# Kernel tuning notes

Measured on AMD Instinct MI355X. Metric: run time of the kernel, lower is better.

The kernel has to match this reference:

```python
import jax, jax.numpy as jnp
import numpy as np

N, E = 50000, 800000
D, DE = 128, 64
BN_EPS = 1e-5


def _bn(h, gamma, beta):
    # BatchNorm1d in training mode: biased batch statistics over the node axis
    mu = jnp.mean(h, axis=0)
    var = jnp.var(h, axis=0)
    return (h - mu) * jax.lax.rsqrt(var + BN_EPS) * gamma + beta


def setup_inputs() -> dict:
    key = jax.random.key(0)
    ks = jax.random.split(key, 12)
    s = lambda d: 1.0 / np.sqrt(d)
    return {
        "x": jax.random.normal(ks[0], (N, D), jnp.float32),
        "edge_index": jax.random.randint(ks[1], (2, E), 0, N, jnp.int64),
        "edge_attr_processed": jax.random.normal(ks[2], (E, DE), jnp.float32),
        # GINEConv edge linear: edge_dim -> node_dim
        "We": jax.random.uniform(ks[3], (D, DE), jnp.float32, -s(DE), s(DE)),
        "be": jnp.zeros((D,), jnp.float32),
        # MLP: Linear(D, 2D) -> BN(2D) -> ReLU -> Linear(2D, D)
        "W1": jax.random.uniform(ks[4], (2 * D, D), jnp.float32, -s(D), s(D)),
        "b1": jnp.zeros((2 * D,), jnp.float32),
        "g1": jnp.ones((2 * D,), jnp.float32),
        "beta1": jnp.zeros((2 * D,), jnp.float32),
        "W2": jax.random.uniform(ks[5], (D, 2 * D), jnp.float32, -s(2 * D), s(2 * D)),
        "b2": jnp.zeros((D,), jnp.float32),
        # outer BatchNorm(D)
        "g2": jnp.ones((D,), jnp.float32),
        "beta2": jnp.zeros((D,), jnp.float32),
        # GINE trainable eps (init 0.0)
        "eps": jnp.zeros((), jnp.float32),
    }


def reference(x, edge_index, edge_attr_processed, We, be, W1, b1, g1, beta1,
              W2, b2, g2, beta2, eps):
    src, dst = edge_index[0], edge_index[1]
    # GINEConv message: ReLU(x_j + Lin(edge_attr)); gather + edge add + relu
    msg = jax.nn.relu(x[src] + edge_attr_processed @ We.T + be)  # [E, D]
    # scatter-add aggregation at destination nodes
    agg = jax.ops.segment_sum(msg, dst, num_segments=x.shape[0])  # [N, D]
    h = (1.0 + eps) * x + agg
    # MLP: Linear -> BN -> ReLU -> Linear
    h = jax.nn.relu(_bn(h @ W1.T + b1, g1, beta1)) @ W2.T + b2
    # outer BN -> ReLU (dropout is identity at inference)
    return jax.nn.relu(_bn(h, g2, beta2))
```

## Files before the change

### kernel.cpp

```cpp
#include <hip/hip_runtime.h>
#include <stdint.h>
#include <stddef.h>


#define NN 50000
#define EE 800000
#define DD 128
#define DE 64
#define H1 256
#define NGRP 3125

typedef __attribute__((ext_vector_type(8))) short short8;
typedef __attribute__((ext_vector_type(4))) float floatx4;

__device__ __forceinline__ short f2bf(float f) {
    union { float f; uint32_t u; } v; v.f = f;
    return (short)((v.u + 0x7FFFu + ((v.u >> 16) & 1u)) >> 16);
}
__device__ __forceinline__ float bf2f(uint16_t u) {
    union { uint32_t u; float f; } v; v.u = (uint32_t)u << 16;
    return v.f;
}

__global__ __launch_bounds__(256) void swz_kernel(const float* __restrict__ src,
                                                  short* __restrict__ dst,
                                                  int KC, int K, int total) {
    int idx = blockIdx.x * 256 + threadIdx.x;
    if (idx >= total) return;
    int j = idx & 7;
    int lane = (idx >> 3) & 63;
    int f = idx >> 9;
    int kc = f % KC;
    int nt = f / KC;
    int n = nt * 16 + (lane & 15);
    int k = kc * 32 + ((lane >> 4) & 3) * 8 + j;
    dst[idx] = f2bf(src[(size_t)n * K + k]);
}

__global__ __launch_bounds__(256) void count_kernel(const int* __restrict__ ei,
                                                    uint32_t* __restrict__ deg) {
    int e = blockIdx.x * 256 + threadIdx.x;
    atomicAdd(&deg[ei[EE + e]], 1u);
}

__global__ __launch_bounds__(256) void scan1_kernel(const uint32_t* __restrict__ deg,
                                                    uint32_t* __restrict__ partial) {
    __shared__ uint32_t ls[256];
    int i = blockIdx.x * 256 + threadIdx.x;
    ls[threadIdx.x] = (i < NN) ? deg[i] : 0u;
    __syncthreads();
    for (int s = 128; s > 0; s >>= 1) {
        if (threadIdx.x < s) ls[threadIdx.x] += ls[threadIdx.x + s];
        __syncthreads();
    }
    if (threadIdx.x == 0) partial[blockIdx.x] = ls[0];
}

__global__ __launch_bounds__(256) void scan2_kernel(uint32_t* __restrict__ partial) {
    __shared__ uint32_t ls[196];
    if (threadIdx.x < 196) ls[threadIdx.x] = partial[threadIdx.x];
    __syncthreads();
    if (threadIdx.x == 0) {
        uint32_t run = 0;
        for (int i = 0; i < 196; ++i) { uint32_t t = ls[i]; ls[i] = run; run += t; }
    }
    __syncthreads();
    if (threadIdx.x < 196) partial[threadIdx.x] = ls[threadIdx.x];
}

__global__ __launch_bounds__(256) void scan3_kernel(const uint32_t* __restrict__ deg,
                                                    const uint32_t* __restrict__ partial,
                                                    uint32_t* __restrict__ base,
                                                    uint32_t* __restrict__ cursor) {
    __shared__ uint32_t ls[256];
    int i = blockIdx.x * 256 + threadIdx.x;
    uint32_t v = (i < NN) ? deg[i] : 0u;
    ls[threadIdx.x] = v;
    __syncthreads();
    for (int off = 1; off < 256; off <<= 1) {
        uint32_t t = (threadIdx.x >= off) ? ls[threadIdx.x - off] : 0u;
        __syncthreads();
        ls[threadIdx.x] += t;
        __syncthreads();
    }
    if (i < NN) {
        uint32_t b = partial[blockIdx.x] + ls[threadIdx.x] - v;
        base[i] = b;
        cursor[i] = b;
    }
}

__global__ __launch_bounds__(256) void pos_kernel(const int* __restrict__ ei,
                                                  uint32_t* __restrict__ cursor,
                                                  uint32_t* __restrict__ pos) {
    int e = blockIdx.x * 256 + threadIdx.x;
    pos[e] = atomicAdd(&cursor[ei[EE + e]], 1u);
}

#define EDGE_GPW 5
__global__ __launch_bounds__(256) void edge_kernel(
    const float* __restrict__ x,
    const int* __restrict__ ei,
    const float* __restrict__ ea,
    const short* __restrict__ weswz,
    const float* __restrict__ be,
    const uint32_t* __restrict__ pos,
    uint16_t* __restrict__ msg)
{
    const int wave = threadIdx.x >> 6;
    const int lane = threadIdx.x & 63;
    const int l16 = lane & 15;
    const int q = lane >> 4;

    const short8* wp = (const short8*)weswz;
    short8 bfr[16];
#pragma unroll
    for (int f = 0; f < 16; ++f) bfr[f] = wp[f * 64 + lane];
    float bev[8];
#pragma unroll
    for (int t = 0; t < 8; ++t) bev[t] = be[t * 16 + l16];

    const int gbase = (blockIdx.x * 4 + wave) * EDGE_GPW;
    for (int g = 0; g < EDGE_GPW; ++g) {
        const int e0 = (gbase + g) * 16;
        const float* earow = ea + (size_t)(e0 + l16) * DE + q * 8;
        floatx4 p0 = *(const floatx4*)(earow);
        floatx4 p1 = *(const floatx4*)(earow + 4);
        floatx4 p2 = *(const floatx4*)(earow + 32);
        floatx4 p3 = *(const floatx4*)(earow + 36);
        short8 af0, af1;
#pragma unroll
        for (int j = 0; j < 4; ++j) {
            af0[j]     = f2bf(p0[j]);
            af0[j + 4] = f2bf(p1[j]);
            af1[j]     = f2bf(p2[j]);
            af1[j + 4] = f2bf(p3[j]);
        }
        floatx4 acc[8];
#pragma unroll
        for (int t = 0; t < 8; ++t) {
            floatx4 z = {0.f, 0.f, 0.f, 0.f};
            z = __builtin_amdgcn_mfma_f32_16x16x32_bf16(af0, bfr[t * 2], z, 0, 0, 0);
            acc[t] = __builtin_amdgcn_mfma_f32_16x16x32_bf16(af1, bfr[t * 2 + 1], z, 0, 0, 0);
        }
#pragma unroll
        for (int r = 0; r < 4; ++r) {
            const int e = e0 + q * 4 + r;
            const int s = ei[e];
            const uint32_t p = pos[e];
            const float* xr = x + (size_t)s * DD;
            uint16_t* mrow = msg + (size_t)p * DD;
#pragma unroll
            for (int t = 0; t < 8; ++t) {
                float v = acc[t][r] + bev[t] + xr[t * 16 + l16];
                v = fmaxf(v, 0.f);
                mrow[t * 16 + l16] = (uint16_t)f2bf(v);
            }
        }
    }
}

__global__ __launch_bounds__(256) void reduce_kernel(
    const uint16_t* __restrict__ msg,
    const uint32_t* __restrict__ base,
    const uint32_t* __restrict__ deg,
    const float* __restrict__ x,
    const float* __restrict__ epsp,
    float* __restrict__ h)
{
    const int n = blockIdx.x * 4 + (threadIdx.x >> 6);
    const int lane = threadIdx.x & 63;
    const uint32_t* mp = (const uint32_t*)msg + (size_t)base[n] * 64 + lane;
    const uint32_t d = deg[n];
    float s0 = 0.f, s1 = 0.f;
    for (uint32_t i = 0; i < d; ++i) {
        uint32_t u = mp[(size_t)i * 64];
        s0 += bf2f((uint16_t)(u & 0xFFFFu));
        s1 += bf2f((uint16_t)(u >> 16));
    }
    const float c1 = 1.0f + epsp[0];
    const int idx = n * DD + lane * 2;
    float2 xv = *(const float2*)(x + idx);
    float2 o; o.x = c1 * xv.x + s0; o.y = c1 * xv.y + s1;
    *(float2*)(h + idx) = o;
}

__global__ __launch_bounds__(256) void gemm1_kernel(
    const float* __restrict__ h,
    const short* __restrict__ w1swz,
    const float* __restrict__ b1,
    float* __restrict__ t1,
    float* __restrict__ gsum,
    float* __restrict__ gsq)
{
    __shared__ float ls[H1];
    __shared__ float ls2[H1];
    const int tid = threadIdx.x;
    ls[tid] = 0.f; ls2[tid] = 0.f;
    __syncthreads();

    const int wave = tid >> 6;
    const int lane = tid & 63;
    const int l16 = lane & 15;
    const int q = lane >> 4;
    const short8* wp = (const short8*)w1swz;

    const int grp = blockIdx.x * 4 + wave;
    if (grp < NGRP) {
        const int n0 = grp * 16;
        const float* hr = h + (size_t)(n0 + l16) * DD + q * 8;
        short8 af[4];
#pragma unroll
        for (int kc = 0; kc < 4; ++kc) {
            floatx4 va = *(const floatx4*)(hr + kc * 32);
            floatx4 vb = *(const floatx4*)(hr + kc * 32 + 4);
#pragma unroll
            for (int j = 0; j < 4; ++j) {
                af[kc][j]     = f2bf(va[j]);
                af[kc][j + 4] = f2bf(vb[j]);
            }
        }
#pragma unroll
        for (int nt = 0; nt < 16; ++nt) {
            floatx4 acc = {0.f, 0.f, 0.f, 0.f};
#pragma unroll
            for (int kc = 0; kc < 4; ++kc)
                acc = __builtin_amdgcn_mfma_f32_16x16x32_bf16(
                    af[kc], wp[(nt * 4 + kc) * 64 + lane], acc, 0, 0, 0);
            const float bb = b1[nt * 16 + l16];
            float s = 0.f, s2 = 0.f;
#pragma unroll
            for (int r = 0; r < 4; ++r) {
                float v = acc[r] + bb;
                t1[(size_t)(n0 + q * 4 + r) * H1 + nt * 16 + l16] = v;
                s += v; s2 += v * v;
            }
            atomicAdd(&ls[nt * 16 + l16], s);
            atomicAdd(&ls2[nt * 16 + l16], s2);
        }
    }
    __syncthreads();
    atomicAdd(&gsum[tid], ls[tid]);
    atomicAdd(&gsq[tid], ls2[tid]);
}

__global__ __launch_bounds__(256) void gemm2_kernel(
    const float* __restrict__ t1,
    const float* __restrict__ scale1,
    const float* __restrict__ shift1,
    const short* __restrict__ w2swz,
    const float* __restrict__ b2,
    float* __restrict__ h2,
    float* __restrict__ gsum,
    float* __restrict__ gsq)
{
    __shared__ float ls[DD];
    __shared__ float ls2[DD];
    const int tid = threadIdx.x;
    if (tid < DD) { ls[tid] = 0.f; ls2[tid] = 0.f; }
    __syncthreads();

    const int wave = tid >> 6;
    const int lane = tid & 63;
    const int l16 = lane & 15;
    const int q = lane >> 4;
    const short8* wp = (const short8*)w2swz;

    const int grp = blockIdx.x * 4 + wave;
    if (grp < NGRP) {
        const int n0 = grp * 16;
        const float* tr = t1 + (size_t)(n0 + l16) * H1 + q * 8;
        floatx4 acc[8];
#pragma unroll
        for (int nt = 0; nt < 8; ++nt) acc[nt] = (floatx4){0.f, 0.f, 0.f, 0.f};
#pragma unroll
        for (int kc = 0; kc < 8; ++kc) {
            floatx4 va = *(const floatx4*)(tr + kc * 32);
            floatx4 vb = *(const floatx4*)(tr + kc * 32 + 4);
            const int kb = kc * 32 + q * 8;
            short8 af;
#pragma unroll
            for (int j = 0; j < 4; ++j) {
                float u = va[j] * scale1[kb + j] + shift1[kb + j];
                af[j] = f2bf(fmaxf(u, 0.f));
                float w = vb[j] * scale1[kb + 4 + j] + shift1[kb + 4 + j];
                af[j + 4] = f2bf(fmaxf(w, 0.f));
            }
#pragma unroll
            for (int nt = 0; nt < 8; ++nt)
                acc[nt] = __builtin_amdgcn_mfma_f32_16x16x32_bf16(
                    af, wp[(nt * 8 + kc) * 64 + lane], acc[nt], 0, 0, 0);
        }
#pragma unroll
        for (int nt = 0; nt < 8; ++nt) {
            const float bb = b2[nt * 16 + l16];
            float s = 0.f, s2 = 0.f;
#pragma unroll
            for (int r = 0; r < 4; ++r) {
                float v = acc[nt][r] + bb;
                h2[(size_t)(n0 + q * 4 + r) * DD + nt * 16 + l16] = v;
                s += v; s2 += v * v;
            }
            atomicAdd(&ls[nt * 16 + l16], s);
            atomicAdd(&ls2[nt * 16 + l16], s2);
        }
    }
    __syncthreads();
    if (tid < DD) {
        atomicAdd(&gsum[tid], ls[tid]);
        atomicAdd(&gsq[tid], ls2[tid]);
    }
}

__global__ void finalize_kernel(const float* __restrict__ ssum,
                                const float* __restrict__ ssumsq,
                                const float* __restrict__ gamma,
                                const float* __restrict__ beta,
                                float* __restrict__ scale,
                                float* __restrict__ shift, int C) {
    int c = threadIdx.x;
    if (c >= C) return;
    float mu = ssum[c] * (1.0f / NN);
    float var = ssumsq[c] * (1.0f / NN) - mu * mu;
    float rs = rsqrtf(var + 1e-5f);
    float sc = gamma[c] * rs;
    scale[c] = sc;
    shift[c] = beta[c] - mu * sc;
}

__global__ __launch_bounds__(256) void out_kernel(const float* __restrict__ h2,
                                                  const float* __restrict__ scale2,
                                                  const float* __restrict__ shift2,
                                                  float* __restrict__ out) {
    int idx = blockIdx.x * 256 + threadIdx.x;
    int base = idx * 4;
    if (base >= NN * DD) return;
    int c = base & (DD - 1);
    floatx4 v = *(const floatx4*)(h2 + base);
    floatx4 sc = *(const floatx4*)(scale2 + c);
    floatx4 sh = *(const floatx4*)(shift2 + c);
    floatx4 o;
#pragma unroll
    for (int j = 0; j < 4; ++j) o[j] = fmaxf(v[j] * sc[j] + sh[j], 0.f);
    *(floatx4*)(out + base) = o;
}

extern "C" void kernel_launch(void* const* d_in, const int* in_sizes, int n_in,
                              void* d_out, int out_size, void* d_ws, size_t ws_size,
                              hipStream_t stream) {
    const float* x     = (const float*)d_in[0];
    const int*   ei    = (const int*)d_in[1];
    const float* ea    = (const float*)d_in[2];
    const float* We    = (const float*)d_in[3];
    const float* be    = (const float*)d_in[4];
    const float* W1    = (const float*)d_in[5];
    const float* b1    = (const float*)d_in[6];
    const float* g1    = (const float*)d_in[7];
    const float* beta1 = (const float*)d_in[8];
    const float* W2    = (const float*)d_in[9];
    const float* b2    = (const float*)d_in[10];
    const float* g2    = (const float*)d_in[11];
    const float* beta2 = (const float*)d_in[12];
    const float* epsp  = (const float*)d_in[13];

    float* ws      = (float*)d_ws;
    float* gsum1   = ws + 0;
    float* gsq1    = ws + 256;
    float* gsum2   = ws + 512;
    float* gsq2    = ws + 640;
    float* scale1  = ws + 768;
    float* shift1  = ws + 1024;
    float* scale2  = ws + 1280;
    float* shift2  = ws + 1408;
    uint32_t* deg     = (uint32_t*)(ws + 1536);
    uint32_t* basep   = deg + 50176;
    uint32_t* cursor  = basep + 50176;
    uint32_t* partial = cursor + 50176;
    uint32_t* pos     = partial + 256;
    float*    h       = (float*)(pos + EE);
    uint16_t* msg     = (uint16_t*)(h + (size_t)NN * DD);
    float*    t1      = (float*)msg;
    float*    h2      = t1 + (size_t)NN * H1;
    short*    weswz   = (short*)(msg + (size_t)EE * DD);
    short*    w1swz   = weswz + 8192;
    short*    w2swz   = w1swz + 32768;

    hipMemsetAsync(ws, 0, (1536 + 50176) * sizeof(uint32_t), stream);

    swz_kernel<<<dim3(32), 256, 0, stream>>>(We, weswz, 2, 64, 8192);
    swz_kernel<<<dim3(128), 256, 0, stream>>>(W1, w1swz, 4, 128, 32768);
    swz_kernel<<<dim3(128), 256, 0, stream>>>(W2, w2swz, 8, 256, 32768);

    count_kernel<<<dim3(3125), 256, 0, stream>>>(ei, deg);
    scan1_kernel<<<dim3(196), 256, 0, stream>>>(deg, partial);
    scan2_kernel<<<dim3(1), 256, 0, stream>>>(partial);
    scan3_kernel<<<dim3(196), 256, 0, stream>>>(deg, partial, basep, cursor);
    pos_kernel<<<dim3(3125), 256, 0, stream>>>(ei, cursor, pos);

    edge_kernel<<<dim3(2500), 256, 0, stream>>>(x, ei, ea, weswz, be, pos, msg);
    reduce_kernel<<<dim3(12500), 256, 0, stream>>>(msg, basep, deg, x, epsp, h);

    gemm1_kernel<<<dim3(782), 256, 0, stream>>>(h, w1swz, b1, t1, gsum1, gsq1);
    finalize_kernel<<<dim3(1), 256, 0, stream>>>(gsum1, gsq1, g1, beta1, scale1, shift1, H1);

    gemm2_kernel<<<dim3(782), 256, 0, stream>>>(t1, scale1, shift1, w2swz, b2, h2, gsum2, gsq2);
    finalize_kernel<<<dim3(1), 128, 0, stream>>>(gsum2, gsq2, g2, beta2, scale2, shift2, DD);

    out_kernel<<<dim3(6250), 256, 0, stream>>>(h2, scale2, shift2, (float*)d_out);
}
```

Before: 699.5 us.

## Fuse edge messages with destination aggregation via CSR order; store intermediates in bf16

The edge kernel now walks edges sorted by destination (a CSR order array) for each group of 16 nodes. It accumulates ReLU messages into a shared-memory tile with LDS atomics and writes h = (1+eps)x + agg directly as bf16. This removes the large E×D bf16 message buffer and the separate reduce pass. The intermediates h, t1 and h2 are also stored in bf16 instead of fp32, and the three weight-swizzle launches are merged into one. The costs are LDS atomic contention, load imbalance from uneven degrees per node group, and extra rounding error from the bf16 intermediates.

```diff
diff --git a/kernel.cpp b/kernel.cpp
--- a/kernel.cpp
+++ b/kernel.cpp
@@ -22,19 +22,23 @@
     return v.f;
 }
 
-__global__ __launch_bounds__(256) void swz_kernel(const float* __restrict__ src,
-                                                  short* __restrict__ dst,
-                                                  int KC, int K, int total) {
+__global__ __launch_bounds__(256) void swz_all_kernel(
+    const float* __restrict__ We, const float* __restrict__ W1,
+    const float* __restrict__ W2, short* __restrict__ dst) {
     int idx = blockIdx.x * 256 + threadIdx.x;
-    if (idx >= total) return;
-    int j = idx & 7;
-    int lane = (idx >> 3) & 63;
-    int f = idx >> 9;
+    if (idx >= 73728) return;
+    const float* src; int KC, K, local; short* dp;
+    if (idx < 8192)       { src = We; KC = 2; K = 64;  local = idx;          dp = dst; }
+    else if (idx < 40960) { src = W1; KC = 4; K = 128; local = idx - 8192;  dp = dst + 8192; }
+    else                  { src = W2; KC = 8; K = 256; local = idx - 40960; dp = dst + 40960; }
+    int j = local & 7;
+    int lane = (local >> 3) & 63;
+    int f = local >> 9;
     int kc = f % KC;
     int nt = f / KC;
     int n = nt * 16 + (lane & 15);
     int k = kc * 32 + ((lane >> 4) & 3) * 8 + j;
-    dst[idx] = f2bf(src[(size_t)n * K + k]);
+    dp[local] = f2bf(src[(size_t)n * K + k]);
 }
 
 __global__ __launch_bounds__(256) void count_kernel(const int* __restrict__ ei,
@@ -47,7 +51,7 @@
                                                     uint32_t* __restrict__ partial) {
     __shared__ uint32_t ls[256];
     int i = blockIdx.x * 256 + threadIdx.x;
-    ls[threadIdx.x] = (i < NN) ? deg[i] : 0u;
+    ls[threadIdx.x] = deg[i];
     __syncthreads();
     for (int s = 128; s > 0; s >>= 1) {
         if (threadIdx.x < s) ls[threadIdx.x] += ls[threadIdx.x + s];
@@ -87,30 +91,38 @@
         uint32_t b = partial[blockIdx.x] + ls[threadIdx.x] - v;
         base[i] = b;
         cursor[i] = b;
-    }
-}
-
-__global__ __launch_bounds__(256) void pos_kernel(const int* __restrict__ ei,
-                                                  uint32_t* __restrict__ cursor,
-                                                  uint32_t* __restrict__ pos) {
+    } else if (i == NN) {
+        base[NN] = EE;
+    }
+}
+
+__global__ __launch_bounds__(256) void order_kernel(const int* __restrict__ ei,
+                                                    uint32_t* __restrict__ cursor,
+                                                    uint32_t* __restrict__ order) {
     int e = blockIdx.x * 256 + threadIdx.x;
-    pos[e] = atomicAdd(&cursor[ei[EE + e]], 1u);
-}
-
-#define EDGE_GPW 5
-__global__ __launch_bounds__(256) void edge_kernel(
+    order[atomicAdd(&cursor[ei[EE + e]], 1u)] = (uint32_t)e;
+}
+
+__global__ __launch_bounds__(256) void edge_agg_kernel(
     const float* __restrict__ x,
     const int* __restrict__ ei,
     const float* __restrict__ ea,
     const short* __restrict__ weswz,
     const float* __restrict__ be,
-    const uint32_t* __restrict__ pos,
-    uint16_t* __restrict__ msg)
+    const uint32_t* __restrict__ order,
+    const uint32_t* __restrict__ basep,
+    const float* __restrict__ epsp,
+    uint16_t* __restrict__ hbf)
 {
+    __shared__ float tile[4][16 * 132];
     const int wave = threadIdx.x >> 6;
     const int lane = threadIdx.x & 63;
     const int l16 = lane & 15;
     const int q = lane >> 4;
+    const int grp = blockIdx.x * 4 + wave;
+    if (grp >= NGRP) return;
+
+    for (int i = lane; i < 16 * 132; i += 64) tile[wave][i] = 0.f;
 
     const short8* wp = (const short8*)weswz;
     short8 bfr[16];
@@ -120,10 +132,15 @@
 #pragma unroll
     for (int t = 0; t < 8; ++t) bev[t] = be[t * 16 + l16];
 
-    const int gbase = (blockIdx.x * 4 + wave) * EDGE_GPW;
-    for (int g = 0; g < EDGE_GPW; ++g) {
-        const int e0 = (gbase + g) * 16;
-        const float* earow = ea + (size_t)(e0 + l16) * DE + q * 8;
+    const int n0 = grp * 16;
+    const int s0 = (int)basep[n0];
+    const int s1 = (int)basep[n0 + 16];
+
+    for (int s = s0; s < s1; s += 16) {
+        int sa = s + l16;
+        if (sa > s1 - 1) sa = s1 - 1;
+        const uint32_t eA = order[sa];
+        const float* earow = ea + (size_t)eA * DE + q * 8;
         floatx4 p0 = *(const floatx4*)(earow);
         floatx4 p1 = *(const floatx4*)(earow + 4);
         floatx4 p2 = *(const floatx4*)(earow + 32);
@@ -145,51 +162,54 @@
         }
 #pragma unroll
         for (int r = 0; r < 4; ++r) {
-            const int e = e0 + q * 4 + r;
-            const int s = ei[e];
-            const uint32_t p = pos[e];
-            const float* xr = x + (size_t)s * DD;
-            uint16_t* mrow = msg + (size_t)p * DD;
-#pragma unroll
-            for (int t = 0; t < 8; ++t) {
-                float v = acc[t][r] + bev[t] + xr[t * 16 + l16];
-                v = fmaxf(v, 0.f);
-                mrow[t * 16 + l16] = (uint16_t)f2bf(v);
+            const int slot = s + q * 4 + r;
+            if (slot < s1) {
+                const uint32_t e = order[slot];
+                const int src = ei[e];
+                const int dl = ei[EE + e] - n0;
+                const float* xr = x + (size_t)src * DD;
+#pragma unroll
+                for (int t = 0; t < 8; ++t) {
+                    float v = acc[t][r] + bev[t] + xr[t * 16 + l16];
+                    v = fmaxf(v, 0.f);
+                    atomicAdd(&tile[wave][dl * 132 + t * 16 + l16], v);
+                }
             }
         }
     }
-}
-
-__global__ __launch_bounds__(256) void reduce_kernel(
-    const uint16_t* __restrict__ msg,
-    const uint32_t* __restrict__ base,
-    const uint32_t* __restrict__ deg,
-    const float* __restrict__ x,
-    const float* __restrict__ epsp,
-    float* __restrict__ h)
-{
-    const int n = blockIdx.x * 4 + (threadIdx.x >> 6);
-    const int lane = threadIdx.x & 63;
-    const uint32_t* mp = (const uint32_t*)msg + (size_t)base[n] * 64 + lane;
-    const uint32_t d = deg[n];
-    float s0 = 0.f, s1 = 0.f;
-    for (uint32_t i = 0; i < d; ++i) {
-        uint32_t u = mp[(size_t)i * 64];
-        s0 += bf2f((uint16_t)(u & 0xFFFFu));
-        s1 += bf2f((uint16_t)(u >> 16));
-    }
+
     const float c1 = 1.0f + epsp[0];
-    const int idx = n * DD + lane * 2;
-    float2 xv = *(const float2*)(x + idx);
-    float2 o; o.x = c1 * xv.x + s0; o.y = c1 * xv.y + s1;
-    *(float2*)(h + idx) = o;
+    const int row = lane >> 2;
+    const int cq = (lane & 3) * 32;
+    const float* xr = x + (size_t)(n0 + row) * DD + cq;
+    uint16_t* hr = hbf + (size_t)(n0 + row) * DD + cq;
+#pragma unroll
+    for (int b = 0; b < 4; ++b) {
+        floatx4 xa = *(const floatx4*)(xr + b * 8);
+        floatx4 xb = *(const floatx4*)(xr + b * 8 + 4);
+        const int off = row * 132 + cq + b * 8;
+        uint32_t pk[4];
+#pragma unroll
+        for (int j = 0; j < 4; ++j) {
+            float v0 = c1 * xa[j] + tile[wave][off + j];
+            float v1 = c1 * xb[j] + tile[wave][off + 4 + j];
+            if (j & 1) {
+                pk[j >> 1]       |= ((uint32_t)(uint16_t)f2bf(v0)) << 16;
+                pk[2 + (j >> 1)] |= ((uint32_t)(uint16_t)f2bf(v1)) << 16;
+            } else {
+                pk[j >> 1]       = (uint32_t)(uint16_t)f2bf(v0);
+                pk[2 + (j >> 1)] = (uint32_t)(uint16_t)f2bf(v1);
+            }
+        }
+        *(uint4*)(hr + b * 8) = make_uint4(pk[0], pk[1], pk[2], pk[3]);
+    }
 }
 
 __global__ __launch_bounds__(256) void gemm1_kernel(
-    const float* __restrict__ h,
+    const uint16_t* __restrict__ hbf,
     const short* __restrict__ w1swz,
     const float* __restrict__ b1,
-    float* __restrict__ t1,
+    uint16_t* __restrict__ t1,
     float* __restrict__ gsum,
     float* __restrict__ gsq)
 {
@@ -208,18 +228,10 @@
     const int grp = blockIdx.x * 4 + wave;
     if (grp < NGRP) {
         const int n0 = grp * 16;
-        const float* hr = h + (size_t)(n0 + l16) * DD + q * 8;
+        const uint16_t* hr = hbf + (size_t)(n0 + l16) * DD + q * 8;
         short8 af[4];
 #pragma unroll
-        for (int kc = 0; kc < 4; ++kc) {
-            floatx4 va = *(const floatx4*)(hr + kc * 32);
-            floatx4 vb = *(const floatx4*)(hr + kc * 32 + 4);
-#pragma unroll
-            for (int j = 0; j < 4; ++j) {
-                af[kc][j]     = f2bf(va[j]);
-                af[kc][j + 4] = f2bf(vb[j]);
-            }
-        }
+        for (int kc = 0; kc < 4; ++kc) af[kc] = *(const short8*)(hr + kc * 32);
 #pragma unroll
         for (int nt = 0; nt < 16; ++nt) {
             floatx4 acc = {0.f, 0.f, 0.f, 0.f};
@@ -232,7 +244,7 @@
 #pragma unroll
             for (int r = 0; r < 4; ++r) {
                 float v = acc[r] + bb;
-                t1[(size_t)(n0 + q * 4 + r) * H1 + nt * 16 + l16] = v;
+                t1[(size_t)(n0 + q * 4 + r) * H1 + nt * 16 + l16] = (uint16_t)f2bf(v);
                 s += v; s2 += v * v;
             }
             atomicAdd(&ls[nt * 16 + l16], s);
@@ -245,12 +257,12 @@
 }
 
 __global__ __launch_bounds__(256) void gemm2_kernel(
-    const float* __restrict__ t1,
+    const uint16_t* __restrict__ t1,
     const float* __restrict__ scale1,
     const float* __restrict__ shift1,
     const short* __restrict__ w2swz,
     const float* __restrict__ b2,
-    float* __restrict__ h2,
+    uint16_t* __restrict__ h2,
     float* __restrict__ gsum,
     float* __restrict__ gsq)
 {
@@ -269,22 +281,19 @@
     const int grp = blockIdx.x * 4 + wave;
     if (grp < NGRP) {
         const int n0 = grp * 16;
-        const float* tr = t1 + (size_t)(n0 + l16) * H1 + q * 8;
+        const uint16_t* tr = t1 + (size_t)(n0 + l16) * H1 + q * 8;
         floatx4 acc[8];
 #pragma unroll
         for (int nt = 0; nt < 8; ++nt) acc[nt] = (floatx4){0.f, 0.f, 0.f, 0.f};
 #pragma unroll
         for (int kc = 0; kc < 8; ++kc) {
-            floatx4 va = *(const floatx4*)(tr + kc * 32);
-            floatx4 vb = *(const floatx4*)(tr + kc * 32 + 4);
+            short8 tv = *(const short8*)(tr + kc * 32);
             const int kb = kc * 32 + q * 8;
             short8 af;
 #pragma unroll
-            for (int j = 0; j < 4; ++j) {
-                float u = va[j] * scale1[kb + j] + shift1[kb + j];
+            for (int j = 0; j < 8; ++j) {
+                float u = bf2f((uint16_t)tv[j]) * scale1[kb + j] + shift1[kb + j];
                 af[j] = f2bf(fmaxf(u, 0.f));
-                float w = vb[j] * scale1[kb + 4 + j] + shift1[kb + 4 + j];
-                af[j + 4] = f2bf(fmaxf(w, 0.f));
             }
 #pragma unroll
             for (int nt = 0; nt < 8; ++nt)
@@ -298,7 +307,7 @@
 #pragma unroll
             for (int r = 0; r < 4; ++r) {
                 float v = acc[nt][r] + bb;
-                h2[(size_t)(n0 + q * 4 + r) * DD + nt * 16 + l16] = v;
+                h2[(size_t)(n0 + q * 4 + r) * DD + nt * 16 + l16] = (uint16_t)f2bf(v);
                 s += v; s2 += v * v;
             }
             atomicAdd(&ls[nt * 16 + l16], s);
@@ -328,21 +337,28 @@
     shift[c] = beta[c] - mu * sc;
 }
 
-__global__ __launch_bounds__(256) void out_kernel(const float* __restrict__ h2,
+__global__ __launch_bounds__(256) void out_kernel(const uint16_t* __restrict__ h2,
                                                   const float* __restrict__ scale2,
                                                   const float* __restrict__ shift2,
                                                   float* __restrict__ out) {
     int idx = blockIdx.x * 256 + threadIdx.x;
-    int base = idx * 4;
-    if (base >= NN * DD) return;
+    int base = idx * 8;
     int c = base & (DD - 1);
-    floatx4 v = *(const floatx4*)(h2 + base);
-    floatx4 sc = *(const floatx4*)(scale2 + c);
-    floatx4 sh = *(const floatx4*)(shift2 + c);
-    floatx4 o;
-#pragma unroll
-    for (int j = 0; j < 4; ++j) o[j] = fmaxf(v[j] * sc[j] + sh[j], 0.f);
-    *(floatx4*)(out + base) = o;
+    uint4 pk = *(const uint4*)(h2 + base);
+    const uint32_t u[4] = {pk.x, pk.y, pk.z, pk.w};
+    floatx4 o0, o1;
+#pragma unroll
+    for (int j = 0; j < 4; ++j) {
+        float vlo = bf2f((uint16_t)(u[j] & 0xFFFFu));
+        float vhi = bf2f((uint16_t)(u[j] >> 16));
+        int cc = c + j * 2;
+        float a = fmaxf(vlo * scale2[cc] + shift2[cc], 0.f);
+        float b = fmaxf(vhi * scale2[cc + 1] + shift2[cc + 1], 0.f);
+        if (j < 2) { o0[j * 2] = a; o0[j * 2 + 1] = b; }
+        else       { o1[(j - 2) * 2] = a; o1[(j - 2) * 2 + 1] = b; }
+    }
+    *(floatx4*)(out + base) = o0;
+    *(floatx4*)(out + base + 4) = o1;
 }
 
 extern "C" void kernel_launch(void* const* d_in, const int* in_sizes, int n_in,
@@ -374,37 +390,34 @@
     float* shift2  = ws + 1408;
     uint32_t* deg     = (uint32_t*)(ws + 1536);
     uint32_t* basep   = deg + 50176;
-    uint32_t* cursor  = basep + 50176;
+    uint32_t* cursor  = basep + 50432;
     uint32_t* partial = cursor + 50176;
-    uint32_t* pos     = partial + 256;
-    float*    h       = (float*)(pos + EE);
-    uint16_t* msg     = (uint16_t*)(h + (size_t)NN * DD);
-    float*    t1      = (float*)msg;
-    float*    h2      = t1 + (size_t)NN * H1;
-    short*    weswz   = (short*)(msg + (size_t)EE * DD);
-    short*    w1swz   = weswz + 8192;
-    short*    w2swz   = w1swz + 32768;
+    uint32_t* order   = partial + 256;
+    uint16_t* hbf     = (uint16_t*)(order + EE);
+    uint16_t* t1      = hbf + (size_t)NN * DD;
+    uint16_t* h2      = t1 + (size_t)NN * H1;
+    short*    wswz    = (short*)(h2 + (size_t)NN * DD);
+    short*    weswz   = wswz;
+    short*    w1swz   = wswz + 8192;
+    short*    w2swz   = wswz + 40960;
 
     hipMemsetAsync(ws, 0, (1536 + 50176) * sizeof(uint32_t), stream);
 
-    swz_kernel<<<dim3(32), 256, 0, stream>>>(We, weswz, 2, 64, 8192);
-    swz_kernel<<<dim3(128), 256, 0, stream>>>(W1, w1swz, 4, 128, 32768);
-    swz_kernel<<<dim3(128), 256, 0, stream>>>(W2, w2swz, 8, 256, 32768);
-
+    swz_all_kernel<<<dim3(288), 256, 0, stream>>>(We, W1, W2, wswz);
     count_kernel<<<dim3(3125), 256, 0, stream>>>(ei, deg);
     scan1_kernel<<<dim3(196), 256, 0, stream>>>(deg, partial);
     scan2_kernel<<<dim3(1), 256, 0, stream>>>(partial);
     scan3_kernel<<<dim3(196), 256, 0, stream>>>(deg, partial, basep, cursor);
-    pos_kernel<<<dim3(3125), 256, 0, stream>>>(ei, cursor, pos);
-
-    edge_kernel<<<dim3(2500), 256, 0, stream>>>(x, ei, ea, weswz, be, pos, msg);
-    reduce_kernel<<<dim3(12500), 256, 0, stream>>>(msg, basep, deg, x, epsp, h);
-
-    gemm1_kernel<<<dim3(782), 256, 0, stream>>>(h, w1swz, b1, t1, gsum1, gsq1);
+    order_kernel<<<dim3(3125), 256, 0, stream>>>(ei, cursor, order);
+
+    edge_agg_kernel<<<dim3(782), 256, 0, stream>>>(x, ei, ea, weswz, be, order,
+                                                   basep, epsp, hbf);
+
+    gemm1_kernel<<<dim3(782), 256, 0, stream>>>(hbf, w1swz, b1, t1, gsum1, gsq1);
     finalize_kernel<<<dim3(1), 256, 0, stream>>>(gsum1, gsq1, g1, beta1, scale1, shift1, H1);
 
     gemm2_kernel<<<dim3(782), 256, 0, stream>>>(t1, scale1, shift1, w2swz, b2, h2, gsum2, gsq2);
     finalize_kernel<<<dim3(1), 128, 0, stream>>>(gsum2, gsq2, g2, beta2, scale2, shift2, DD);
 
-    out_kernel<<<dim3(6250), 256, 0, stream>>>(h2, scale2, shift2, (float*)d_out);
-}
+    out_kernel<<<dim3(3125), 256, 0, stream>>>(h2, scale2, shift2, (float*)d_out);
+}
```

Measured after the change: 1.154 ms. 1.65x slower.
